# Performance work log

Hardware: AMD Instinct MI355X
Metric: run time of the kernel (lower is better)

The kernel has to match this reference:

```python
import jax, jax.numpy as jnp
import numpy as np

E, D, A, EMB, V = 2048, 512, 512, 512, 10000  # encoder_dim, decoder_dim, attention_dim, embed_dim, vocab


def setup_inputs() -> dict:
    key = jax.random.key(0)
    ks = jax.random.split(key, 20)
    s = 0.02
    B, P, T = 64, 196, 40
    return {
        "encoder_out": jax.random.normal(ks[0], (B, P, E), jnp.float32),
        "captions": jax.random.randint(ks[1], (B, T), 0, V),
        "caption_lengths": jax.random.randint(ks[2], (B,), 1, T),
        "enc_att_W": jax.random.normal(ks[3], (E, A)) * s,
        "enc_att_b": jnp.zeros((A,)),
        "dec_att_W": jax.random.normal(ks[4], (D, A)) * s,
        "dec_att_b": jnp.zeros((A,)),
        "full_att_W": jax.random.normal(ks[5], (A,)) * s,
        "full_att_b": jnp.zeros(()),
        "embedding": jax.random.normal(ks[6], (V, EMB)) * s,
        "W_ih": jax.random.normal(ks[7], (EMB + E, 4 * D)) * s,
        "b_ih": jnp.zeros((4 * D,)),
        "W_hh": jax.random.normal(ks[8], (D, 4 * D)) * s,
        "b_hh": jnp.zeros((4 * D,)),
        "init_h_W": jax.random.normal(ks[9], (E, D)) * s,
        "init_h_b": jnp.zeros((D,)),
        "init_c_W": jax.random.normal(ks[10], (E, D)) * s,
        "init_c_b": jnp.zeros((D,)),
        "fc_W": jax.random.normal(ks[11], (D, V)) * s,
        "fc_b": jnp.zeros((V,)),
        "f_beta_W": jax.random.normal(ks[12], (D, E)) * s,
        "f_beta_b": jnp.zeros((E,)),
    }


def reference(encoder_out, captions, caption_lengths,
              enc_att_W, enc_att_b, dec_att_W, dec_att_b, full_att_W, full_att_b,
              embedding, W_ih, b_ih, W_hh, b_hh,
              init_h_W, init_h_b, init_c_W, init_c_b,
              fc_W, fc_b, f_beta_W, f_beta_b):
    # init hidden state from mean-pooled encoder features
    mean_enc = encoder_out.mean(axis=1)                      # [B, E]
    h = mean_enc @ init_h_W + init_h_b                       # [B, D]
    c = mean_enc @ init_c_W + init_c_b

    embs = embedding[captions]                               # [B, T, EMB]
    # encoder_att(encoder_out) is step-invariant -> precompute once
    att1 = jnp.einsum('bpe,ea->bpa', encoder_out, enc_att_W) + enc_att_b  # [B, P, A]

    def step(carry, emb_t):
        h, c = carry
        att2 = h @ dec_att_W + dec_att_b                     # [B, A]
        e = jax.nn.relu(att1 + att2[:, None, :]) @ full_att_W + full_att_b  # [B, P]
        alpha = jax.nn.softmax(e, axis=1)                    # [B, P]
        context = jnp.einsum('bpe,bp->be', encoder_out, alpha)  # [B, E]
        gate = jax.nn.sigmoid(h @ f_beta_W + f_beta_b)       # [B, E]
        x = jnp.concatenate([emb_t, gate * context], axis=1)  # [B, EMB+E]
        gates = x @ W_ih + b_ih + h @ W_hh + b_hh            # [B, 4D]
        i, f, g, o = jnp.split(gates, 4, axis=1)
        c_new = jax.nn.sigmoid(f) * c + jax.nn.sigmoid(i) * jnp.tanh(g)
        h_new = jax.nn.sigmoid(o) * jnp.tanh(c_new)
        preds = h_new @ fc_W + fc_b                          # [B, V] (dropout = identity at eval)
        return (h_new, c_new), (preds, alpha)

    (_, _), (preds_t, alphas_t) = jax.lax.scan(step, (h, c), jnp.swapaxes(embs, 0, 1))
    predictions = jnp.swapaxes(preds_t, 0, 1)                # [B, T, V]
    alphas = jnp.swapaxes(alphas_t, 0, 1)                    # [B, T, P]
    return predictions, alphas
```

## Files before the change

### kernel.cpp

```cpp
#include <hip/hip_runtime.h>
#include <cstdint>
#include <cstddef>

#define B_   64
#define P_   196
#define E_   2048
#define A_   512
#define D_   512
#define EMB_ 512
#define V_   10000
#define T_   40
#define NCAT  14608
#define NCATP 14656

typedef unsigned short u16;
typedef __attribute__((ext_vector_type(8))) short bf16x8;
typedef __attribute__((ext_vector_type(4))) float f32x4;

__device__ __forceinline__ f32x4 mfma_bf16(bf16x8 a, bf16x8 b, f32x4 c) {
  return __builtin_amdgcn_mfma_f32_16x16x32_bf16(a, b, c, 0, 0, 0);
}
__device__ __forceinline__ u16 f2b(float f) {
  unsigned u = __builtin_bit_cast(unsigned, f);
  u += 0x7fffu + ((u >> 16) & 1u);
  return (u16)(u >> 16);
}
__device__ __forceinline__ float b2f(u16 s) {
  unsigned u = ((unsigned)s) << 16;
  return __builtin_bit_cast(float, u);
}
__device__ __forceinline__ float sigf(float x) { return 1.0f / (1.0f + __expf(-x)); }

__global__ __launch_bounds__(256) void k_cvt_bf16(const float* __restrict__ s,
                                                  u16* __restrict__ d, int n4) {
  int i = blockIdx.x * 256 + threadIdx.x;
  if (i >= n4) return;
  float4 v = reinterpret_cast<const float4*>(s)[i];
  u16* o = d + (size_t)i * 4;
  o[0] = f2b(v.x); o[1] = f2b(v.y); o[2] = f2b(v.z); o[3] = f2b(v.w);
}

__global__ __launch_bounds__(256) void k_mean(const float* __restrict__ enc,
                                              float* __restrict__ meanE) {
  int i = blockIdx.x * 256 + threadIdx.x;
  int b = i >> 11, e = i & 2047;
  const float* p = enc + (size_t)b * P_ * E_ + e;
  float s = 0.f;
  for (int pp = 0; pp < P_; ++pp) s += p[(size_t)pp * E_];
  meanE[i] = s * (1.0f / (float)P_);
}

__global__ __launch_bounds__(256) void k_transpose_bf16(
    const float* __restrict__ src, int srcStride,
    u16* __restrict__ dst, int dstStride, int N, int K) {
  __shared__ float t[32][33];
  int kt = blockIdx.x * 32, nt = blockIdx.y * 32;
  int tx = threadIdx.x & 31, ty = threadIdx.x >> 5;
  #pragma unroll
  for (int i = 0; i < 4; ++i) {
    int k = kt + ty + i * 8, n = nt + tx;
    t[ty + i * 8][tx] = (k < K && n < N) ? src[(size_t)k * srcStride + n] : 0.0f;
  }
  __syncthreads();
  #pragma unroll
  for (int i = 0; i < 4; ++i) {
    int n = nt + ty + i * 8, k = kt + tx;
    if (n < N && k < K) dst[(size_t)n * dstStride + k] = f2b(t[tx][ty + i * 8]);
  }
}

__global__ __launch_bounds__(256) void k_init_hc(
    const float* __restrict__ meanE,
    const float* __restrict__ Wh, const float* __restrict__ bh,
    const float* __restrict__ Wc, const float* __restrict__ bc,
    u16* __restrict__ h_bf, float* __restrict__ c_f) {
  int i = blockIdx.x * 256 + threadIdx.x;
  int b = i >> 9, n = i & 511;
  const float* m = meanE + (size_t)b * E_;
  float ah = 0.f, ac = 0.f;
  for (int k = 0; k < E_; ++k) {
    float mv = m[k];
    ah += mv * Wh[(size_t)k * D_ + n];
    ac += mv * Wc[(size_t)k * D_ + n];
  }
  h_bf[i] = f2b(ah + bh[n]);
  c_f[i]  = ac + bc[n];
}

__global__ __launch_bounds__(256) void k_emb(const int* __restrict__ captions,
                                             const float* __restrict__ embedding,
                                             u16* __restrict__ embs) {
  int i = blockIdx.x * 256 + threadIdx.x;
  int m = i >> 9, k = i & 511;
  int t = m >> 6, b = m & 63;
  int cap = captions[b * T_ + t];
  embs[i] = f2b(embedding[(size_t)cap * EMB_ + k]);
}

__global__ __launch_bounds__(256) void k_bsum(const float* __restrict__ a,
                                              const float* __restrict__ b,
                                              float* __restrict__ o) {
  int i = blockIdx.x * 256 + threadIdx.x;
  o[i] = a[i] + b[i];
}

template <bool BF16OUT>
__global__ __launch_bounds__(256) void k_gemm_bt(
    const u16* __restrict__ Am, const u16* __restrict__ Bt,
    const float* __restrict__ bias, void* __restrict__ outp, int K, int N) {
  int m0 = blockIdx.x * 64, n0 = blockIdx.y * 64;
  int w = threadIdx.x >> 6, lane = threadIdx.x & 63;
  int lr = lane & 15, lg = lane >> 4;
  const u16* ap = Am + (size_t)(m0 + 16 * w + lr) * K + lg * 8;
  const u16* bp = Bt + (size_t)(n0 + lr) * K + lg * 8;
  f32x4 acc0 = {}, acc1 = {}, acc2 = {}, acc3 = {};
  for (int k = 0; k < K; k += 32) {
    bf16x8 a  = *reinterpret_cast<const bf16x8*>(ap + k);
    bf16x8 b0 = *reinterpret_cast<const bf16x8*>(bp + k);
    bf16x8 b1 = *reinterpret_cast<const bf16x8*>(bp + (size_t)16 * K + k);
    bf16x8 b2 = *reinterpret_cast<const bf16x8*>(bp + (size_t)32 * K + k);
    bf16x8 b3 = *reinterpret_cast<const bf16x8*>(bp + (size_t)48 * K + k);
    acc0 = mfma_bf16(a, b0, acc0);
    acc1 = mfma_bf16(a, b1, acc1);
    acc2 = mfma_bf16(a, b2, acc2);
    acc3 = mfma_bf16(a, b3, acc3);
  }
  int row = m0 + 16 * w + 4 * lg;
  f32x4 accs[4] = {acc0, acc1, acc2, acc3};
  #pragma unroll
  for (int ns = 0; ns < 4; ++ns) {
    int col = n0 + 16 * ns + lr;
    float bv = bias[col];
    #pragma unroll
    for (int r = 0; r < 4; ++r) {
      float v = accs[ns][r] + bv;
      if (BF16OUT) ((u16*)outp)[(size_t)(row + r) * N + col] = f2b(v);
      else         ((float*)outp)[(size_t)(row + r) * N + col] = v;
    }
  }
}

__global__ __launch_bounds__(256) void k_stepA(
    const u16* __restrict__ h_bf, const u16* __restrict__ catW,
    const float* __restrict__ dec_b, const float* __restrict__ fbeta_b,
    const float* __restrict__ fc_b, const float* __restrict__ embW_t,
    float* __restrict__ att2, float* __restrict__ gate,
    float* __restrict__ gates, float* __restrict__ preds, int wp) {
  int n0 = blockIdx.x * 64;
  int w = threadIdx.x >> 6, lane = threadIdx.x & 63;
  int lr = lane & 15, lg = lane >> 4;
  const u16* ap = h_bf + (size_t)(16 * w + lr) * 512 + lg * 8;
  const u16* bp = catW + (size_t)(n0 + lr) * 512 + lg * 8;
  f32x4 acc0 = {}, acc1 = {}, acc2 = {}, acc3 = {};
  for (int k = 0; k < 512; k += 32) {
    bf16x8 a  = *reinterpret_cast<const bf16x8*>(ap + k);
    bf16x8 b0 = *reinterpret_cast<const bf16x8*>(bp + k);
    bf16x8 b1 = *reinterpret_cast<const bf16x8*>(bp + (size_t)16 * 512 + k);
    bf16x8 b2 = *reinterpret_cast<const bf16x8*>(bp + (size_t)32 * 512 + k);
    bf16x8 b3 = *reinterpret_cast<const bf16x8*>(bp + (size_t)48 * 512 + k);
    acc0 = mfma_bf16(a, b0, acc0);
    acc1 = mfma_bf16(a, b1, acc1);
    acc2 = mfma_bf16(a, b2, acc2);
    acc3 = mfma_bf16(a, b3, acc3);
  }
  int brow = 16 * w + 4 * lg;
  f32x4 accs[4] = {acc0, acc1, acc2, acc3};
  #pragma unroll
  for (int ns = 0; ns < 4; ++ns) {
    int n = n0 + 16 * ns + lr;
    #pragma unroll
    for (int r = 0; r < 4; ++r) {
      int b = brow + r;
      float v = accs[ns][r];
      if (n < 512) {
        att2[b * 512 + n] = v + dec_b[n];
      } else if (n < 2560) {
        int j = n - 512;
        gate[b * 2048 + j] = sigf(v + fbeta_b[j]);
      } else if (n < 4608) {
        int j = n - 2560;
        gates[b * 2048 + j] = v + embW_t[b * 2048 + j];
      } else if (n < 14608) {
        int j = n - 4608;
        if (wp) preds[(size_t)b * (T_ * V_) + j] = v + fc_b[j];
      }
    }
  }
}

__global__ __launch_bounds__(256) void k_stepB(
    const u16* __restrict__ att1, const float* __restrict__ att2,
    const float* __restrict__ wf, const float* __restrict__ bf_,
    float* __restrict__ e) {
  int unit = blockIdx.x * 4 + (threadIdx.x >> 6);
  int lane = threadIdx.x & 63;
  int b = unit / 196;
  const u16*  a1  = att1 + (size_t)unit * 512 + lane * 8;
  const float* a2 = att2 + b * 512 + lane * 8;
  const float* wv = wf + lane * 8;
  float s = 0.f;
  #pragma unroll
  for (int j = 0; j < 8; ++j) {
    float x = b2f(a1[j]) + a2[j];
    s += fmaxf(x, 0.f) * wv[j];
  }
  #pragma unroll
  for (int off = 32; off > 0; off >>= 1) s += __shfl_xor(s, off);
  if (lane == 0) e[unit] = s + bf_[0];
}

__global__ __launch_bounds__(256) void k_stepD(
    const float* __restrict__ e, const u16* __restrict__ enc_bf,
    const float* __restrict__ gate, float* __restrict__ alphas,
    u16* __restrict__ gctx) {
  __shared__ float sal[P_];
  __shared__ float red[256];
  int b = blockIdx.x >> 3, ch = blockIdx.x & 7;
  int tid = threadIdx.x;
  float ev = (tid < P_) ? e[b * P_ + tid] : -1e30f;
  red[tid] = ev; __syncthreads();
  for (int s = 128; s > 0; s >>= 1) {
    if (tid < s) red[tid] = fmaxf(red[tid], red[tid + s]);
    __syncthreads();
  }
  float mx = red[0]; __syncthreads();
  float ex = (tid < P_) ? __expf(ev - mx) : 0.f;
  red[tid] = ex; __syncthreads();
  for (int s = 128; s > 0; s >>= 1) {
    if (tid < s) red[tid] += red[tid + s];
    __syncthreads();
  }
  float inv = 1.0f / red[0];
  if (tid < P_) {
    float al = ex * inv;
    sal[tid] = al;
    if (ch == 0) alphas[(size_t)b * (T_ * P_) + tid] = al;
  }
  __syncthreads();
  int eidx = ch * 256 + tid;
  const u16* ep = enc_bf + (size_t)b * P_ * E_ + eidx;
  float acc = 0.f;
  #pragma unroll 4
  for (int p = 0; p < P_; ++p) acc += sal[p] * b2f(ep[(size_t)p * E_]);
  gctx[b * E_ + eidx] = f2b(acc * gate[b * E_ + eidx]);
}

__global__ __launch_bounds__(256) void k_stepE1(
    const u16* __restrict__ gctx, const u16* __restrict__ Wt,
    float* __restrict__ gates) {
  int n0 = (blockIdx.x & 31) * 64;
  int k0 = (blockIdx.x >> 5) * 256;
  int w = threadIdx.x >> 6, lane = threadIdx.x & 63;
  int lr = lane & 15, lg = lane >> 4;
  const u16* ap = gctx + (size_t)(16 * w + lr) * 2048 + lg * 8 + k0;
  const u16* bp = Wt + (size_t)(n0 + lr) * 2048 + lg * 8 + k0;
  f32x4 acc0 = {}, acc1 = {}, acc2 = {}, acc3 = {};
  for (int k = 0; k < 256; k += 32) {
    bf16x8 a  = *reinterpret_cast<const bf16x8*>(ap + k);
    bf16x8 b0 = *reinterpret_cast<const bf16x8*>(bp + k);
    bf16x8 b1 = *reinterpret_cast<const bf16x8*>(bp + (size_t)16 * 2048 + k);
    bf16x8 b2 = *reinterpret_cast<const bf16x8*>(bp + (size_t)32 * 2048 + k);
    bf16x8 b3 = *reinterpret_cast<const bf16x8*>(bp + (size_t)48 * 2048 + k);
    acc0 = mfma_bf16(a, b0, acc0);
    acc1 = mfma_bf16(a, b1, acc1);
    acc2 = mfma_bf16(a, b2, acc2);
    acc3 = mfma_bf16(a, b3, acc3);
  }
  int brow = 16 * w + 4 * lg;
  f32x4 accs[4] = {acc0, acc1, acc2, acc3};
  #pragma unroll
  for (int ns = 0; ns < 4; ++ns) {
    int n = n0 + 16 * ns + lr;
    #pragma unroll
    for (int r = 0; r < 4; ++r)
      atomicAdd(&gates[(brow + r) * 2048 + n], accs[ns][r]);
  }
}

__global__ __launch_bounds__(256) void k_stepE2(
    const float* __restrict__ gates, float* __restrict__ c, u16* __restrict__ h_bf) {
  int i = blockIdx.x * 256 + threadIdx.x;
  int b = i >> 9, d = i & 511;
  const float* g = gates + (size_t)b * 2048;
  float gi = g[d], gf = g[d + 512], gg = g[d + 1024], go = g[d + 1536];
  float cn = sigf(gf) * c[i] + sigf(gi) * tanhf(gg);
  float hn = sigf(go) * tanhf(cn);
  c[i] = cn;
  h_bf[i] = f2b(hn);
}

extern "C" void kernel_launch(void* const* d_in, const int* in_sizes, int n_in,
                              void* d_out, int out_size, void* d_ws, size_t ws_size,
                              hipStream_t stream) {
  (void)in_sizes; (void)n_in; (void)out_size;
  const float* enc        = (const float*)d_in[0];
  const int*   captions   = (const int*)d_in[1];
  const float* enc_att_W  = (const float*)d_in[3];
  const float* enc_att_b  = (const float*)d_in[4];
  const float* dec_att_W  = (const float*)d_in[5];
  const float* dec_att_b  = (const float*)d_in[6];
  const float* full_att_W = (const float*)d_in[7];
  const float* full_att_b = (const float*)d_in[8];
  const float* embedding  = (const float*)d_in[9];
  const float* W_ih       = (const float*)d_in[10];
  const float* b_ih       = (const float*)d_in[11];
  const float* W_hh       = (const float*)d_in[12];
  const float* b_hh       = (const float*)d_in[13];
  const float* init_h_W   = (const float*)d_in[14];
  const float* init_h_b   = (const float*)d_in[15];
  const float* init_c_W   = (const float*)d_in[16];
  const float* init_c_b   = (const float*)d_in[17];
  const float* fc_W       = (const float*)d_in[18];
  const float* fc_b       = (const float*)d_in[19];
  const float* f_beta_W   = (const float*)d_in[20];
  const float* f_beta_b   = (const float*)d_in[21];

  float* preds_out  = (float*)d_out;
  float* alphas_out = (float*)d_out + (size_t)B_ * T_ * V_;

  char* w = (char*)d_ws;
  auto alloc = [&](size_t bytes) -> char* {
    char* p = w; w += (bytes + 255) & ~(size_t)255; return p;
  };
  u16*   enc_bf   = (u16*)  alloc((size_t)B_ * P_ * E_ * 2);
  u16*   att1_bf  = (u16*)  alloc((size_t)B_ * P_ * A_ * 2);
  u16*   catW     = (u16*)  alloc((size_t)NCATP * 512 * 2);
  u16*   encattWT = (u16*)  alloc((size_t)A_ * E_ * 2);
  u16*   WihembT  = (u16*)  alloc((size_t)2048 * 512 * 2);
  u16*   Wih2T    = (u16*)  alloc((size_t)2048 * 2048 * 2);
  u16*   embs_bf  = (u16*)  alloc((size_t)T_ * B_ * EMB_ * 2);
  float* embW     = (float*)alloc((size_t)(T_ + 1) * B_ * 2048 * 4);
  float* meanE    = (float*)alloc((size_t)B_ * E_ * 4);
  u16*   h_bf     = (u16*)  alloc((size_t)B_ * D_ * 2);
  float* c_f      = (float*)alloc((size_t)B_ * D_ * 4);
  float* att2_f   = (float*)alloc((size_t)B_ * A_ * 4);
  float* gate_f   = (float*)alloc((size_t)B_ * E_ * 4);
  float* gates_f  = (float*)alloc((size_t)B_ * 2048 * 4);
  float* e_f      = (float*)alloc((size_t)B_ * P_ * 4);
  u16*   gctx_bf  = (u16*)  alloc((size_t)B_ * E_ * 2);
  float* bsum     = (float*)alloc(2048 * 4);
  if ((size_t)(w - (char*)d_ws) > ws_size) return;

  k_cvt_bf16<<<25088, 256, 0, stream>>>(enc, enc_bf, (B_ * P_ * E_) / 4);
  k_mean<<<512, 256, 0, stream>>>(enc, meanE);
  k_transpose_bf16<<<dim3(16, 16), 256, 0, stream>>>(dec_att_W, 512, catW, 512, 512, 512);
  k_transpose_bf16<<<dim3(16, 64), 256, 0, stream>>>(f_beta_W, 2048, catW + (size_t)512 * 512, 512, 2048, 512);
  k_transpose_bf16<<<dim3(16, 64), 256, 0, stream>>>(W_hh, 2048, catW + (size_t)2560 * 512, 512, 2048, 512);
  k_transpose_bf16<<<dim3(16, 313), 256, 0, stream>>>(fc_W, 10000, catW + (size_t)4608 * 512, 512, 10000, 512);
  hipMemsetAsync(catW + (size_t)NCAT * 512, 0, (size_t)(NCATP - NCAT) * 512 * 2, stream);
  k_transpose_bf16<<<dim3(64, 16), 256, 0, stream>>>(enc_att_W, 512, encattWT, 2048, 512, 2048);
  k_transpose_bf16<<<dim3(16, 64), 256, 0, stream>>>(W_ih, 2048, WihembT, 512, 2048, 512);
  k_transpose_bf16<<<dim3(64, 64), 256, 0, stream>>>(W_ih + (size_t)512 * 2048, 2048, Wih2T, 2048, 2048, 2048);
  k_bsum<<<8, 256, 0, stream>>>(b_ih, b_hh, bsum);
  k_init_hc<<<128, 256, 0, stream>>>(meanE, init_h_W, init_h_b, init_c_W, init_c_b, h_bf, c_f);
  k_emb<<<5120, 256, 0, stream>>>(captions, embedding, embs_bf);
  k_gemm_bt<true><<<dim3(196, 8), 256, 0, stream>>>(enc_bf, encattWT, enc_att_b, att1_bf, 2048, 512);
  k_gemm_bt<false><<<dim3(40, 32), 256, 0, stream>>>(embs_bf, WihembT, bsum, embW, 512, 2048);

  for (int t = 0; t <= T_; ++t) {
    int tm1 = t - 1;
    float* preds = preds_out + (size_t)(tm1 < 0 ? 0 : tm1) * V_;
    k_stepA<<<NCATP / 64, 256, 0, stream>>>(h_bf, catW, dec_att_b, f_beta_b, fc_b,
                                            embW + (size_t)t * B_ * 2048,
                                            att2_f, gate_f, gates_f, preds, tm1 >= 0 ? 1 : 0);
    if (t == T_) break;
    k_stepB<<<3136, 256, 0, stream>>>(att1_bf, att2_f, full_att_W, full_att_b, e_f);
    k_stepD<<<512, 256, 0, stream>>>(e_f, enc_bf, gate_f, alphas_out + (size_t)t * P_, gctx_bf);
    k_stepE1<<<256, 256, 0, stream>>>(gctx_bf, Wih2T, gates_f);
    k_stepE2<<<128, 256, 0, stream>>>(gates_f, c_f, h_bf);
  }
}
```

Measured before the change: 2.860 ms.

## Use MFMA GEMMs for init h/c and LDS-tiled 128x128 prologue GEMMs

Replaces the scalar fp32 init_hc kernel with a bf16 MFMA GEMM over concatenated transposed init_h/init_c weights, then unpacks the result into h and c. Adds a 128x128 LDS-tiled GEMM that loads tiles with global_load_lds and reuses them across waves, used for the att1 and embedding-projection prologue GEMMs. This targets the slow naive init kernel and the low-reuse 64x64 direct-load GEMMs, at the cost of extra transpose launches and bf16 rounding of the mean features.

```diff
diff --git a/kernel.cpp b/kernel.cpp
--- a/kernel.cpp
+++ b/kernel.cpp
@@ -31,6 +31,13 @@
 }
 __device__ __forceinline__ float sigf(float x) { return 1.0f / (1.0f + __expf(-x)); }
 
+__device__ __forceinline__ void gl_lds16(const u16* gsrc, u16* ldst) {
+  __builtin_amdgcn_global_load_lds(
+      (const __attribute__((address_space(1))) unsigned int*)gsrc,
+      (__attribute__((address_space(3))) unsigned int*)ldst,
+      16, 0, 0);
+}
+
 __global__ __launch_bounds__(256) void k_cvt_bf16(const float* __restrict__ s,
                                                   u16* __restrict__ d, int n4) {
   int i = blockIdx.x * 256 + threadIdx.x;
@@ -41,13 +48,13 @@
 }
 
 __global__ __launch_bounds__(256) void k_mean(const float* __restrict__ enc,
-                                              float* __restrict__ meanE) {
+                                              u16* __restrict__ meanE_bf) {
   int i = blockIdx.x * 256 + threadIdx.x;
   int b = i >> 11, e = i & 2047;
   const float* p = enc + (size_t)b * P_ * E_ + e;
   float s = 0.f;
   for (int pp = 0; pp < P_; ++pp) s += p[(size_t)pp * E_];
-  meanE[i] = s * (1.0f / (float)P_);
+  meanE_bf[i] = f2b(s * (1.0f / (float)P_));
 }
 
 __global__ __launch_bounds__(256) void k_transpose_bf16(
@@ -69,24 +76,6 @@
   }
 }
 
-__global__ __launch_bounds__(256) void k_init_hc(
-    const float* __restrict__ meanE,
-    const float* __restrict__ Wh, const float* __restrict__ bh,
-    const float* __restrict__ Wc, const float* __restrict__ bc,
-    u16* __restrict__ h_bf, float* __restrict__ c_f) {
-  int i = blockIdx.x * 256 + threadIdx.x;
-  int b = i >> 9, n = i & 511;
-  const float* m = meanE + (size_t)b * E_;
-  float ah = 0.f, ac = 0.f;
-  for (int k = 0; k < E_; ++k) {
-    float mv = m[k];
-    ah += mv * Wh[(size_t)k * D_ + n];
-    ac += mv * Wc[(size_t)k * D_ + n];
-  }
-  h_bf[i] = f2b(ah + bh[n]);
-  c_f[i]  = ac + bc[n];
-}
-
 __global__ __launch_bounds__(256) void k_emb(const int* __restrict__ captions,
                                              const float* __restrict__ embedding,
                                              u16* __restrict__ embs) {
@@ -102,6 +91,22 @@
                                               float* __restrict__ o) {
   int i = blockIdx.x * 256 + threadIdx.x;
   o[i] = a[i] + b[i];
+}
+
+__global__ __launch_bounds__(256) void k_catbias(const float* __restrict__ hb,
+                                                 const float* __restrict__ cb,
+                                                 float* __restrict__ o) {
+  int i = blockIdx.x * 256 + threadIdx.x;
+  o[i] = (i < 512) ? hb[i] : cb[i - 512];
+}
+
+__global__ __launch_bounds__(256) void k_hc_pack(const float* __restrict__ initHC,
+                                                 u16* __restrict__ h_bf,
+                                                 float* __restrict__ c_f) {
+  int i = blockIdx.x * 256 + threadIdx.x;
+  int b = i >> 9, d = i & 511;
+  h_bf[i] = f2b(initHC[b * 1024 + d]);
+  c_f[i]  = initHC[b * 1024 + 512 + d];
 }
 
 template <bool BF16OUT>
@@ -136,6 +141,61 @@
       float v = accs[ns][r] + bv;
       if (BF16OUT) ((u16*)outp)[(size_t)(row + r) * N + col] = f2b(v);
       else         ((float*)outp)[(size_t)(row + r) * N + col] = v;
+    }
+  }
+}
+
+template <bool BF16OUT>
+__global__ __launch_bounds__(256) void k_gemm128(
+    const u16* __restrict__ Am, const u16* __restrict__ Bt,
+    const float* __restrict__ bias, void* __restrict__ outp, int K, int N) {
+  __shared__ u16 lA[128 * 64];
+  __shared__ u16 lB[128 * 64];
+  int n0 = blockIdx.x * 128, m0 = blockIdx.y * 128;
+  int w = threadIdx.x >> 6, lane = threadIdx.x & 63;
+  int wr = w >> 1, wc = w & 1;
+  int lr = lane & 15, lg = lane >> 4;
+  int srow = lane >> 3;
+  int scol = (lane & 7) * 8;
+  f32x4 acc[4][4] = {};
+  for (int kt = 0; kt < K; kt += 64) {
+    #pragma unroll
+    for (int q = 0; q < 4; ++q) {
+      int r = (w * 4 + q) * 8 + srow;
+      gl_lds16(Am + (size_t)(m0 + r) * K + kt + scol, &lA[(w * 4 + q) * 512]);
+      gl_lds16(Bt + (size_t)(n0 + r) * K + kt + scol, &lB[(w * 4 + q) * 512]);
+    }
+    __syncthreads();
+    #pragma unroll
+    for (int kk = 0; kk < 2; ++kk) {
+      bf16x8 af[4], bf[4];
+      #pragma unroll
+      for (int m = 0; m < 4; ++m)
+        af[m] = *reinterpret_cast<const bf16x8*>(&lA[(wr * 64 + m * 16 + lr) * 64 + kk * 32 + lg * 8]);
+      #pragma unroll
+      for (int n = 0; n < 4; ++n)
+        bf[n] = *reinterpret_cast<const bf16x8*>(&lB[(wc * 64 + n * 16 + lr) * 64 + kk * 32 + lg * 8]);
+      #pragma unroll
+      for (int m = 0; m < 4; ++m)
+        #pragma unroll
+        for (int n = 0; n < 4; ++n)
+          acc[m][n] = mfma_bf16(af[m], bf[n], acc[m][n]);
+    }
+    __syncthreads();
+  }
+  #pragma unroll
+  for (int n = 0; n < 4; ++n) {
+    int col = n0 + wc * 64 + n * 16 + lr;
+    float bv = bias[col];
+    #pragma unroll
+    for (int m = 0; m < 4; ++m) {
+      int row = m0 + wr * 64 + m * 16 + lg * 4;
+      #pragma unroll
+      for (int r = 0; r < 4; ++r) {
+        float v = acc[m][n][r] + bv;
+        if (BF16OUT) ((u16*)outp)[(size_t)(row + r) * N + col] = f2b(v);
+        else         ((float*)outp)[(size_t)(row + r) * N + col] = v;
+      }
     }
   }
 }
@@ -330,7 +390,10 @@
   u16*   Wih2T    = (u16*)  alloc((size_t)2048 * 2048 * 2);
   u16*   embs_bf  = (u16*)  alloc((size_t)T_ * B_ * EMB_ * 2);
   float* embW     = (float*)alloc((size_t)(T_ + 1) * B_ * 2048 * 4);
-  float* meanE    = (float*)alloc((size_t)B_ * E_ * 4);
+  u16*   catInit  = (u16*)  alloc((size_t)1024 * 2048 * 2);
+  float* catInitB = (float*)alloc(1024 * 4);
+  float* initHC   = (float*)alloc((size_t)B_ * 1024 * 4);
+  u16*   meanE_bf = (u16*)  alloc((size_t)B_ * E_ * 2);
   u16*   h_bf     = (u16*)  alloc((size_t)B_ * D_ * 2);
   float* c_f      = (float*)alloc((size_t)B_ * D_ * 4);
   float* att2_f   = (float*)alloc((size_t)B_ * A_ * 4);
@@ -342,7 +405,7 @@
   if ((size_t)(w - (char*)d_ws) > ws_size) return;
 
   k_cvt_bf16<<<25088, 256, 0, stream>>>(enc, enc_bf, (B_ * P_ * E_) / 4);
-  k_mean<<<512, 256, 0, stream>>>(enc, meanE);
+  k_mean<<<512, 256, 0, stream>>>(enc, meanE_bf);
   k_transpose_bf16<<<dim3(16, 16), 256, 0, stream>>>(dec_att_W, 512, catW, 512, 512, 512);
   k_transpose_bf16<<<dim3(16, 64), 256, 0, stream>>>(f_beta_W, 2048, catW + (size_t)512 * 512, 512, 2048, 512);
   k_transpose_bf16<<<dim3(16, 64), 256, 0, stream>>>(W_hh, 2048, catW + (size_t)2560 * 512, 512, 2048, 512);
@@ -351,11 +414,15 @@
   k_transpose_bf16<<<dim3(64, 16), 256, 0, stream>>>(enc_att_W, 512, encattWT, 2048, 512, 2048);
   k_transpose_bf16<<<dim3(16, 64), 256, 0, stream>>>(W_ih, 2048, WihembT, 512, 2048, 512);
   k_transpose_bf16<<<dim3(64, 64), 256, 0, stream>>>(W_ih + (size_t)512 * 2048, 2048, Wih2T, 2048, 2048, 2048);
+  k_transpose_bf16<<<dim3(64, 16), 256, 0, stream>>>(init_h_W, 512, catInit, 2048, 512, 2048);
+  k_transpose_bf16<<<dim3(64, 16), 256, 0, stream>>>(init_c_W, 512, catInit + (size_t)512 * 2048, 2048, 512, 2048);
+  k_catbias<<<4, 256, 0, stream>>>(init_h_b, init_c_b, catInitB);
   k_bsum<<<8, 256, 0, stream>>>(b_ih, b_hh, bsum);
-  k_init_hc<<<128, 256, 0, stream>>>(meanE, init_h_W, init_h_b, init_c_W, init_c_b, h_bf, c_f);
   k_emb<<<5120, 256, 0, stream>>>(captions, embedding, embs_bf);
-  k_gemm_bt<true><<<dim3(196, 8), 256, 0, stream>>>(enc_bf, encattWT, enc_att_b, att1_bf, 2048, 512);
-  k_gemm_bt<false><<<dim3(40, 32), 256, 0, stream>>>(embs_bf, WihembT, bsum, embW, 512, 2048);
+  k_gemm_bt<false><<<dim3(1, 16), 256, 0, stream>>>(meanE_bf, catInit, catInitB, initHC, 2048, 1024);
+  k_hc_pack<<<128, 256, 0, stream>>>(initHC, h_bf, c_f);
+  k_gemm128<true><<<dim3(4, 98), 256, 0, stream>>>(enc_bf, encattWT, enc_att_b, att1_bf, 2048, 512);
+  k_gemm128<false><<<dim3(16, 20), 256, 0, stream>>>(embs_bf, WihembT, bsum, embW, 512, 2048);
 
   for (int t = 0; t <= T_; ++t) {
     int tm1 = t - 1;
```

New measurement: 2.558 ms. 10.6% less time.
